# Performance work log

Measured on AMD Instinct MI355X. Metric: run time of the kernel, lower is better.

## Reference

```python
import jax, jax.numpy as jnp
import numpy as np

CODEBOOK_SIZE = 4096
CODE_DIM = 256
N = 65536
COMMITMENT_COST = 0.25


def setup_inputs() -> dict:
    key = jax.random.key(0)
    k1, k2 = jax.random.split(key)
    z_flat = jax.random.normal(k1, (N, CODE_DIM), dtype=jnp.float32)
    # embedding initialized uniform(-1/codebook_size, 1/codebook_size) as in torch module
    emb_weight = jax.random.uniform(
        k2, (CODEBOOK_SIZE, CODE_DIM), dtype=jnp.float32,
        minval=-1.0 / CODEBOOK_SIZE, maxval=1.0 / CODEBOOK_SIZE)
    return {"z_flat": z_flat, "emb_weight": emb_weight}


def reference(z_flat, emb_weight):
    # squared L2 distances: [N, K] = |z|^2 + |e|^2 - 2 z e^T
    distances = (
        jnp.sum(z_flat ** 2, axis=1, keepdims=True)
        + jnp.sum(emb_weight ** 2, axis=1)
        - 2.0 * jnp.matmul(z_flat, emb_weight.T)
    )
    indices = jnp.argmin(distances, axis=1)  # [N]
    quantized = emb_weight[indices]          # [N, code_dim]

    e_latent_loss = jnp.mean((jax.lax.stop_gradient(quantized) - z_flat) ** 2)
    q_latent_loss = jnp.mean((quantized - jax.lax.stop_gradient(z_flat)) ** 2)
    loss = q_latent_loss + COMMITMENT_COST * e_latent_loss

    # straight-through estimator
    quantized_st = z_flat + jax.lax.stop_gradient(quantized - z_flat)
    return (loss, quantized_st, indices)
```

## Files before the change

kernel.cpp:

```cpp
#include <hip/hip_runtime.h>

#define KCODES 4096
#define DIM    256
#define NROWS  65536
#define MARGIN 4.0e-4f
#define DSLACK 4.0e-5f
#define QDELT  4.0e-5f
#define LCAP   4096
#define CPAD   32
#define LSTRIDE (DIM + 4)

typedef unsigned long long u64;
typedef unsigned int  uint;
typedef unsigned short ushort;
typedef __attribute__((ext_vector_type(8))) short bf16x8;
typedef __attribute__((ext_vector_type(4))) float f32x4;

typedef __attribute__((address_space(3))) uint lds_u32_t;
typedef __attribute__((address_space(1))) uint glb_u32_t;

__device__ __forceinline__ void g2lds16(const void* g, void* l) {
    __builtin_amdgcn_global_load_lds((const glb_u32_t*)g, (lds_u32_t*)l, 16, 0, 0);
}

__device__ __forceinline__ float dppmin_pair(float m) {
    m = fminf(m, __int_as_float(__builtin_amdgcn_update_dpp(0, __float_as_int(m), 0xB1, 0xF, 0xF, true)));
    return m;
}
__device__ __forceinline__ float dppmin_row16(float m) {
    m = fminf(m, __int_as_float(__builtin_amdgcn_update_dpp(0, __float_as_int(m), 0xB1, 0xF, 0xF, true)));
    m = fminf(m, __int_as_float(__builtin_amdgcn_update_dpp(0, __float_as_int(m), 0x4E, 0xF, 0xF, true)));
    m = fminf(m, __int_as_float(__builtin_amdgcn_update_dpp(0, __float_as_int(m), 0x124, 0xF, 0xF, true)));
    m = fminf(m, __int_as_float(__builtin_amdgcn_update_dpp(0, __float_as_int(m), 0x128, 0xF, 0xF, true)));
    return m;
}
__device__ __forceinline__ uint dppor_row16(uint v) {
    v |= (uint)__builtin_amdgcn_update_dpp(0, (int)v, 0xB1, 0xF, 0xF, true);
    v |= (uint)__builtin_amdgcn_update_dpp(0, (int)v, 0x4E, 0xF, 0xF, true);
    v |= (uint)__builtin_amdgcn_update_dpp(0, (int)v, 0x124, 0xF, 0xF, true);
    v |= (uint)__builtin_amdgcn_update_dpp(0, (int)v, 0x128, 0xF, 0xF, true);
    return v;
}


__device__ __forceinline__ float np_half_sum128(const float4* __restrict__ p4) {
    #pragma clang fp contract(off)
    float4 v0 = p4[0], v1 = p4[1];
    float r0 = v0.x * v0.x, r1 = v0.y * v0.y, r2 = v0.z * v0.z, r3 = v0.w * v0.w;
    float r4 = v1.x * v1.x, r5 = v1.y * v1.y, r6 = v1.z * v1.z, r7 = v1.w * v1.w;
    #pragma unroll
    for (int i = 1; i < 16; ++i) {
        float4 a = p4[2 * i], b = p4[2 * i + 1];
        r0 += a.x * a.x; r1 += a.y * a.y; r2 += a.z * a.z; r3 += a.w * a.w;
        r4 += b.x * b.x; r5 += b.y * b.y; r6 += b.z * b.z; r7 += b.w * b.w;
    }
    return ((r0 + r1) + (r2 + r3)) + ((r4 + r5) + (r6 + r7));
}

__global__ void k_rownorm(const float* __restrict__ src, float* __restrict__ dst, int nrows) {
    int r = blockIdx.x * blockDim.x + threadIdx.x;
    if (r >= nrows) return;
    const float4* p4 = (const float4*)(src + (size_t)r * DIM);
    float s;
    {
        #pragma clang fp contract(off)
        s = np_half_sum128(p4) + np_half_sum128(p4 + 32);
    }
    dst[r] = s;
}

__device__ __forceinline__ float f32_dist(float Cr, float ebc, double accv) {
    #pragma clang fp contract(off)
    float A = Cr + ebc;
    float B = 2.0f * (float)accv;
    return A - B;
}

__device__ __forceinline__ ushort f2bf(float f) {
    uint u = __float_as_uint(f);
    return (ushort)((u + 0x7fffu + ((u >> 16) & 1u)) >> 16);
}

__device__ __forceinline__ uint4 pack8(float4 a, float4 b) {
    uint4 ov;
    ov.x = (uint)f2bf(a.x) | ((uint)f2bf(a.y) << 16);
    ov.y = (uint)f2bf(a.z) | ((uint)f2bf(a.w) << 16);
    ov.z = (uint)f2bf(b.x) | ((uint)f2bf(b.y) << 16);
    ov.w = (uint)f2bf(b.z) | ((uint)f2bf(b.w) << 16);
    return ov;
}


__global__ void k_prep(const float* __restrict__ src, ushort* __restrict__ dst,
                       float* __restrict__ nrm, int nrows) {
    int r = blockIdx.x * blockDim.x + threadIdx.x;
    if (r >= nrows) return;
    const float4* p4 = (const float4*)(src + (size_t)r * DIM);
    uint4* d4 = (uint4*)(dst + (size_t)r * DIM);
    float h[2];
    #pragma unroll
    for (int half = 0; half < 2; ++half) {
        #pragma clang fp contract(off)
        const float4* p = p4 + half * 32;
        float4 v0 = p[0], v1 = p[1];
        d4[half * 16] = pack8(v0, v1);
        float r0 = v0.x * v0.x, r1 = v0.y * v0.y, r2 = v0.z * v0.z, r3 = v0.w * v0.w;
        float r4 = v1.x * v1.x, r5 = v1.y * v1.y, r6 = v1.z * v1.z, r7 = v1.w * v1.w;
        #pragma unroll
        for (int i = 1; i < 16; ++i) {
            float4 a = p[2 * i], b = p[2 * i + 1];
            d4[half * 16 + i] = pack8(a, b);
            r0 += a.x * a.x; r1 += a.y * a.y; r2 += a.z * a.z; r3 += a.w * a.w;
            r4 += b.x * b.x; r5 += b.y * b.y; r6 += b.z * b.z; r7 += b.w * b.w;
        }
        h[half] = ((r0 + r1) + (r2 + r3)) + ((r4 + r5) + (r6 + r7));
    }
    {
        #pragma clang fp contract(off)
        nrm[r] = h[0] + h[1];
    }
}

__global__ void k_init(int* __restrict__ cnt) {
    cnt[blockIdx.x * 256 + threadIdx.x] = 0;
}

__global__ __launch_bounds__(256, 2)
void k_gemm(const ushort* __restrict__ zh, const ushort* __restrict__ eh,
            const float* __restrict__ Crow, const float* __restrict__ eb2,
            float* __restrict__ tk, uint* __restrict__ tk2) {
    __shared__ __align__(16) ushort Bs[2][64 * 256];

    const int t = threadIdx.x;
    const int lane = t & 63;
    const int w = t >> 6;
    const int l15 = lane & 15, l4 = lane >> 4;
    const int row0w = blockIdx.x * 128 + w * 32;

    const char* ebp = (const char*)eh;

    auto stage = [&](int buf, int ct2) {
        const char* base = ebp + (size_t)ct2 * 64 * 512;
        #pragma unroll
        for (int i = 0; i < 8; ++i) {
            int idx = i * 256 + t;
            int code = idx >> 5;
            int c16  = idx & 31;
            int src  = (code << 9) + ((c16 ^ (code & 7)) << 4);
            g2lds16(base + src, (char*)Bs[buf] + idx * 16);
        }
    };

    bf16x8 a[2][8];
    #pragma unroll
    for (int f = 0; f < 2; ++f)
        #pragma unroll
        for (int ks = 0; ks < 8; ++ks)
            a[f][ks] = *(const bf16x8*)&zh[(size_t)(row0w + f * 16 + l15) * 256 + ks * 32 + l4 * 8];

    float crf[8];
    #pragma unroll
    for (int f = 0; f < 2; ++f)
        #pragma unroll
        for (int rg = 0; rg < 4; ++rg)
            crf[f * 4 + rg] = Crow[row0w + f * 16 + l4 * 4 + rg];

    float mprev[8];
    const f32x4 fzero = (f32x4){0.f, 0.f, 0.f, 0.f};
    f32x4 accA[2][4], accB[2][4];
    float ebvA[4], ebvB[4];

    auto ksloop = [&](const ushort* Bb, f32x4 (&acc)[2][4]) {
        #pragma unroll
        for (int ks = 0; ks < 8; ++ks) {
            bf16x8 bfv[4];
            #pragma unroll
            for (int cg = 0; cg < 4; ++cg) {
                int rB = cg * 16 + l15;
                int off = rB * 256 + ((ks * 32 + l4 * 8) ^ ((l15 & 7) << 3));
                bfv[cg] = *(const bf16x8*)&Bb[off];
            }
            __builtin_amdgcn_s_setprio(1);
            #pragma unroll
            for (int f = 0; f < 2; ++f)
                #pragma unroll
                for (int cg = 0; cg < 4; ++cg)
                    acc[f][cg] = __builtin_amdgcn_mfma_f32_16x16x32_bf16(
                        a[f][ks], bfv[cg], ks == 0 ? fzero : acc[f][cg], 0, 0, 0);
            __builtin_amdgcn_s_setprio(0);
        }
    };

    auto epi = [&](f32x4 (&acc)[2][4], const float (&ebv)[4], int ct2, bool odd) {
        #pragma unroll
        for (int f = 0; f < 2; ++f) {
            #pragma unroll
            for (int rg = 0; rg < 4; ++rg) {
                float m =    fmaf(-2.0f, acc[f][0][rg], ebv[0]);
                m = fminf(m, fmaf(-2.0f, acc[f][1][rg], ebv[1]));
                m = fminf(m, fmaf(-2.0f, acc[f][2][rg], ebv[2]));
                m = fminf(m, fmaf(-2.0f, acc[f][3][rg], ebv[3]));
                m = dppmin_pair(m);
                if (!odd) {
                    mprev[f * 4 + rg] = m;
                } else {
                    m = fminf(m, mprev[f * 4 + rg]);
                    float mt = dppmin_row16(m);
                    int q = (int)((m - mt) * 2.5e4f);
                    q = q > 15 ? 15 : q;
                    uint pk = (uint)q << (4 * (l15 >> 1));
                    pk = dppor_row16(pk);
                    if (l15 == 0) {
                        int grow = row0w + f * 16 + l4 * 4 + rg;
                        int tt = ct2 >> 1;
                        tk [(size_t)tt * NROWS + grow] = crf[f * 4 + rg] + mt;
                        tk2[(size_t)tt * NROWS + grow] = pk;
                    }
                }
            }
        }
    };

    stage(0, 0);
    #pragma unroll
    for (int cg = 0; cg < 4; ++cg) ebvA[cg] = eb2[cg * 16 + l15];
    __syncthreads();

    for (int tp = 0; tp < 32; ++tp) {
        int t0 = 2 * tp;
        stage(1, t0 + 1);
        if (tp > 0) epi(accB, ebvB, t0 - 1, true);
        ksloop(Bs[0], accA);
        __syncthreads();

        if (tp < 31) stage(0, t0 + 2);
        #pragma unroll
        for (int cg = 0; cg < 4; ++cg) ebvB[cg] = eb2[(t0 + 1) * 64 + cg * 16 + l15];
        epi(accA, ebvA, t0, false);
        if (tp < 31) {
            #pragma unroll
            for (int cg = 0; cg < 4; ++cg) ebvA[cg] = eb2[(t0 + 2) * 64 + cg * 16 + l15];
        }
        ksloop(Bs[1], accB);
        __syncthreads();
    }
    epi(accB, ebvB, 63, true);
}

__global__ void k_lists(const float* __restrict__ tk, const uint* __restrict__ tk2,
                        int* __restrict__ cnt, int* __restrict__ list,
                        u64* __restrict__ fkey) {
    int row = blockIdx.x * 256 + threadIdx.x;
    int lane = threadIdx.x & 63;
    float tm[32]; uint pk[32];
    #pragma unroll
    for (int tt = 0; tt < 32; ++tt) {
        tm[tt] = tk [(size_t)tt * NROWS + row];
        pk[tt] = tk2[(size_t)tt * NROWS + row];
    }
    float best = tm[0];
    #pragma unroll
    for (int tt = 1; tt < 32; ++tt) best = fminf(best, tm[tt]);
    fkey[row] = ~0ull;
    float cutoff = best + (MARGIN + DSLACK);

    #pragma unroll
    for (int tt = 0; tt < 32; ++tt) {
        #pragma unroll
        for (int p = 0; p < 8; ++p) {
            float v = tm[tt] + (float)((pk[tt] >> (4 * p)) & 15u) * QDELT;
            bool pred = v <= cutoff;
            u64 mask = __ballot(pred);
            if (mask) {
                int sub = tt * 8 + p;
                int nq = __popcll(mask);
                int rank = __popcll(mask & ((1ull << lane) - 1ull));
                int base = 0;
                if (lane == 0) base = atomicAdd(&cnt[sub * CPAD], nq);
                base = __shfl(base, 0, 64);
                int pos = base + rank;
                if (pred && pos < LCAP) list[sub * LCAP + pos] = row;
            }
        }
    }
}

__global__ __launch_bounds__(256, 2)
void k_exact(const float* __restrict__ z, const float* __restrict__ e,
             const float* __restrict__ Crow, const float* __restrict__ eb2,
             const int* __restrict__ list, const int* __restrict__ cnt,
             u64* __restrict__ fkey) {
    __shared__ __align__(16) float ex[16][260];
    __shared__ __align__(16) float zx[32][260];
    __shared__ int rows[32];
    __shared__ u64 keytab[32][17];
    const int sub = blockIdx.x;
    const int tile = sub >> 3, p2 = sub & 7;
    const int nct = cnt[sub * CPAD];
    const int t = threadIdx.x;
    const int rp = t & 15, cs = t >> 4;

    {
        int cc = t >> 4, c8 = t & 15;
        int gcode = tile * 128 + (cc >> 3) * 64 + ((cc >> 1) & 3) * 16 + p2 * 2 + (cc & 1);
        const float4* src = (const float4*)(e + (size_t)gcode * DIM);
        float4* dr = (float4*)ex[cc];
        #pragma unroll
        for (int j = 0; j < 4; ++j) dr[c8 + 16 * j] = src[c8 + 16 * j];
    }
    const int gc0 = tile * 128 + (cs >> 3) * 64 + ((cs >> 1) & 3) * 16 + p2 * 2 + (cs & 1);
    const float ebc0 = eb2[gc0];

    for (int base = blockIdx.y * 32; base < nct; base += gridDim.y * 32) {
        __syncthreads();
        if (t < 32) {
            int i = base + t;
            rows[t] = list[sub * LCAP + (i < nct ? i : nct - 1)];
        }
        __syncthreads();
        {
            int rr = t >> 3, c8 = t & 7;
            const float4* src = (const float4*)(z + (size_t)rows[rr] * DIM);
            float4* dr = (float4*)zx[rr];
            #pragma unroll
            for (int j = 0; j < 8; ++j) dr[c8 + 8 * j] = src[c8 + 8 * j];
        }
        __syncthreads();

        double a0 = 0.0, a1 = 0.0;
        const float4* z0 = (const float4*)zx[rp];
        const float4* z1 = (const float4*)zx[rp + 16];
        const float4* e0 = (const float4*)ex[cs];
        #pragma unroll 8
        for (int d4 = 0; d4 < 64; ++d4) {
            float4 x0 = z0[d4], x1 = z1[d4], y0 = e0[d4];
            a0 += (double)x0.x * (double)y0.x; a0 += (double)x0.y * (double)y0.y;
            a0 += (double)x0.z * (double)y0.z; a0 += (double)x0.w * (double)y0.w;
            a1 += (double)x1.x * (double)y0.x; a1 += (double)x1.y * (double)y0.y;
            a1 += (double)x1.z * (double)y0.z; a1 += (double)x1.w * (double)y0.w;
        }
        int r0 = rows[rp], r1 = rows[rp + 16];
        float C0 = Crow[r0], C1 = Crow[r1];
        keytab[rp][cs]      = ((u64)__float_as_uint(f32_dist(C0, ebc0, a0)) << 32) | (u64)gc0;
        keytab[rp + 16][cs] = ((u64)__float_as_uint(f32_dist(C1, ebc0, a1)) << 32) | (u64)gc0;
        __syncthreads();
        if (t < 32) {
            u64 kb = keytab[t][0];
            #pragma unroll
            for (int j = 1; j < 16; ++j) {
                u64 k = keytab[t][j];
                kb = k < kb ? k : kb;
            }
            atomicMin((unsigned long long*)&fkey[rows[t]], kb);
        }
    }
}

__global__ __launch_bounds__(256)
void k_gather(const float* __restrict__ z, const float* __restrict__ e,
              const u64* __restrict__ fkey, float* __restrict__ out,
              double* __restrict__ partial) {
    __shared__ double lred[4];
    const int t = threadIdx.x;
    const int row = blockIdx.x * 32 + (t >> 3);
    const int c8 = t & 7;
    const int idx = (int)(fkey[row] & 0xffffffffull);
    if (c8 == 0) out[1 + (size_t)NROWS * DIM + row] = (float)idx;
    const float4* zr = (const float4*)(z + (size_t)row * DIM);
    const float4* er = (const float4*)(e + (size_t)idx * DIM);
    float4* orow = (float4*)(out + 1 + (size_t)row * DIM);
    double lacc = 0.0;
    #pragma unroll
    for (int j = 0; j < 8; ++j) {
        float4 q = er[c8 + 8 * j];
        float4 zv = zr[c8 + 8 * j];
        orow[c8 + 8 * j] = q;
        double d0 = (double)q.x - (double)zv.x;
        double d1 = (double)q.y - (double)zv.y;
        double d2 = (double)q.z - (double)zv.z;
        double d3 = (double)q.w - (double)zv.w;
        lacc += d0 * d0 + d1 * d1 + d2 * d2 + d3 * d3;
    }
    for (int off = 32; off > 0; off >>= 1) lacc += __shfl_down(lacc, off, 64);
    if ((t & 63) == 0) lred[t >> 6] = lacc;
    __syncthreads();
    if (t == 0) partial[blockIdx.x] = lred[0] + lred[1] + lred[2] + lred[3];
}

__global__ void k_finish(const double* __restrict__ partial, float* __restrict__ out, int n) {
    __shared__ double s[256];
    double a = 0.0;
    for (int i = threadIdx.x; i < n; i += 256) a += partial[i];
    s[threadIdx.x] = a;
    __syncthreads();
    for (int off = 128; off > 0; off >>= 1) {
        if (threadIdx.x < off) s[threadIdx.x] += s[threadIdx.x + off];
        __syncthreads();
    }
    if (threadIdx.x == 0)
        out[0] = (float)(1.25 * s[0] / ((double)NROWS * (double)DIM));
}


__global__ __launch_bounds__(256, 1)
void k_main_slow(const float* __restrict__ z, const float* __restrict__ e,
                 const float* __restrict__ Crow, const float* __restrict__ eb2,
                 float* __restrict__ out, double* __restrict__ partial) {
    __shared__ float  zt[64][LSTRIDE];
    __shared__ float  et[64][LSTRIDE];
    __shared__ float  redd[64][17];
    __shared__ int    redi[64][17];
    __shared__ int    bsel[64];
    __shared__ double lred[4];

    const int t  = threadIdx.x;
    const int tx = t & 15;
    const int ty = t >> 4;
    const int row0 = blockIdx.x * 64;

    {
        const float4* zsrc = (const float4*)(z + (size_t)row0 * DIM);
        for (int i = t; i < 64 * (DIM / 4); i += 256) {
            int r = i >> 6, c4 = i & 63;
            *(float4*)&zt[r][c4 * 4] = zsrc[r * (DIM / 4) + c4];
        }
    }
    float Cr[4];
    #pragma unroll
    for (int ri = 0; ri < 4; ++ri) Cr[ri] = Crow[row0 + ty * 4 + ri];
    float bestd[4]; int besti[4];
    #pragma unroll
    for (int ri = 0; ri < 4; ++ri) { bestd[ri] = __int_as_float(0x7f800000); besti[ri] = 0; }

    for (int kt = 0; kt < KCODES / 64; ++kt) {
        __syncthreads();
        {
            const float4* esrc = (const float4*)(e + (size_t)kt * 64 * DIM);
            for (int i = t; i < 64 * (DIM / 4); i += 256) {
                int r = i >> 6, c4 = i & 63;
                *(float4*)&et[r][c4 * 4] = esrc[r * (DIM / 4) + c4];
            }
        }
        __syncthreads();
        double acc[4][4];
        #pragma unroll
        for (int a = 0; a < 4; ++a)
            #pragma unroll
            for (int b = 0; b < 4; ++b) acc[a][b] = 0.0;
        #pragma unroll 4
        for (int d4 = 0; d4 < DIM / 4; ++d4) {
            float4 za[4], ea[4];
            #pragma unroll
            for (int ri = 0; ri < 4; ++ri) za[ri] = *(const float4*)&zt[ty * 4 + ri][d4 * 4];
            #pragma unroll
            for (int ci = 0; ci < 4; ++ci) ea[ci] = *(const float4*)&et[tx + 16 * ci][d4 * 4];
            #pragma unroll
            for (int ri = 0; ri < 4; ++ri)
                #pragma unroll
                for (int ci = 0; ci < 4; ++ci)
                    acc[ri][ci] += (double)za[ri].x * (double)ea[ci].x
                                 + (double)za[ri].y * (double)ea[ci].y
                                 + (double)za[ri].z * (double)ea[ci].z
                                 + (double)za[ri].w * (double)ea[ci].w;
        }
        #pragma unroll
        for (int ci = 0; ci < 4; ++ci) {
            int c = kt * 64 + tx + 16 * ci;
            float ebc = eb2[c];
            #pragma unroll
            for (int ri = 0; ri < 4; ++ri) {
                float d = f32_dist(Cr[ri], ebc, acc[ri][ci]);
                if (d < bestd[ri]) { bestd[ri] = d; besti[ri] = c; }
            }
        }
    }
    __syncthreads();
    #pragma unroll
    for (int ri = 0; ri < 4; ++ri) {
        redd[ty * 4 + ri][tx] = bestd[ri];
        redi[ty * 4 + ri][tx] = besti[ri];
    }
    __syncthreads();
    if (t < 64) {
        float bd = redd[t][0]; int bi = redi[t][0];
        for (int j = 1; j < 16; ++j) {
            float d = redd[t][j]; int i2 = redi[t][j];
            if (d < bd || (d == bd && i2 < bi)) { bd = d; bi = i2; }
        }
        bsel[t] = bi;
        out[1 + (size_t)NROWS * DIM + row0 + t] = (float)bi;
    }
    __syncthreads();
    double lacc = 0.0;
    {
        int r = t >> 2, qd = (t & 3) * 64;
        int bi = bsel[r];
        const float* qrow = e + (size_t)bi * DIM + qd;
        float* orow = out + 1 + (size_t)(row0 + r) * DIM + qd;
        #pragma unroll 4
        for (int d = 0; d < 64; ++d) {
            float qv = qrow[d], zv = zt[r][qd + d];
            double df = (double)qv - (double)zv;
            lacc += df * df;
            orow[d] = qv;
        }
    }
    for (int off = 32; off > 0; off >>= 1) lacc += __shfl_down(lacc, off, 64);
    if ((t & 63) == 0) lred[t >> 6] = lacc;
    __syncthreads();
    if (t == 0) partial[blockIdx.x] = lred[0] + lred[1] + lred[2] + lred[3];
}


extern "C" void kernel_launch(void* const* d_in, const int* in_sizes, int n_in,
                              void* d_out, int out_size, void* d_ws, size_t ws_size,
                              hipStream_t stream) {
    const float* z = (const float*)d_in[0];
    const float* e = (const float*)d_in[1];
    float* out = (float*)d_out;
    char* w = (char*)d_ws;

    size_t o = 0;
    auto take = [&](size_t b) { size_t r = o; o = (o + b + 255) & ~(size_t)255; return r; };
    size_t o_zh = take((size_t)NROWS * DIM * 2);
    size_t o_eh = take((size_t)KCODES * DIM * 2);
    size_t o_cr = take((size_t)NROWS * 4);
    size_t o_eb = take((size_t)KCODES * 4);
    size_t o_tk = take((size_t)32 * NROWS * 4);
    size_t o_t2 = take((size_t)32 * NROWS * 4);
    size_t o_fk = take((size_t)NROWS * 8);
    size_t o_cn = take((size_t)256 * CPAD * 4);
    size_t o_ls = take((size_t)256 * LCAP * 4);
    size_t o_pt = take((size_t)2048 * 8);
    size_t need = o;

    if (ws_size >= need) {
        ushort* zh = (ushort*)(w + o_zh);
        ushort* eh = (ushort*)(w + o_eh);
        float* Cr  = (float*)(w + o_cr);
        float* eb  = (float*)(w + o_eb);
        float* tk  = (float*)(w + o_tk);
        uint*  tk2 = (uint*)(w + o_t2);
        u64*   fk  = (u64*)(w + o_fk);
        int*   cn  = (int*)(w + o_cn);
        int*   ls  = (int*)(w + o_ls);
        double* pt = (double*)(w + o_pt);

        k_prep<<<NROWS / 256, 256, 0, stream>>>(z, zh, Cr, NROWS);
        k_prep<<<KCODES / 256, 256, 0, stream>>>(e, eh, eb, KCODES);
        k_init<<<(256 * CPAD) / 256, 256, 0, stream>>>(cn);
        k_gemm<<<NROWS / 128, 256, 0, stream>>>(zh, eh, Cr, eb, tk, tk2);
        k_lists<<<NROWS / 256, 256, 0, stream>>>(tk, tk2, cn, ls, fk);
        dim3 ge(256, 8);
        k_exact<<<ge, 256, 0, stream>>>(z, e, Cr, eb, ls, cn, fk);
        k_gather<<<NROWS / 32, 256, 0, stream>>>(z, e, fk, out, pt);
        k_finish<<<1, 256, 0, stream>>>(pt, out, 2048);
    } else {
        float* Cr  = (float*)w;
        float* eb  = Cr + NROWS;
        double* pt = (double*)(eb + KCODES);
        k_rownorm<<<NROWS / 256, 256, 0, stream>>>(z, Cr, NROWS);
        k_rownorm<<<KCODES / 256, 256, 0, stream>>>(e, eb, KCODES);
        k_main_slow<<<NROWS / 64, 256, 0, stream>>>(z, e, Cr, eb, out, pt);
        k_finish<<<1, 256, 0, stream>>>(pt, out, NROWS / 64);
    }
}
```

Baseline: 334.5 us.

## Enlarge exact-rescore row tile and derive loss from stored distances

The exact fp64 rescoring kernel now handles 64 candidate rows per iteration, and each thread computes two codes against two rows, so every z value read from LDS is reused across two codes and the per-row reduction shrinks from 16 entries to 8. Launch bounds drop to one block per SM to leave room for the larger shared tiles and extra accumulators. The gather kernel stops reading z and instead sums the winning distance stored in the key's upper 32 bits to form the loss, which removes a full pass over z and the fp64 difference arithmetic. The trade-off is that the loss now rests on the float32 f32_dist value rather than an exact fp64 recomputation, and occupancy in the rescoring kernel is lower.

```diff
diff --git a/kernel.cpp b/kernel.cpp
--- a/kernel.cpp
+++ b/kernel.cpp
@@ -285,69 +285,83 @@
     }
 }
 
-__global__ __launch_bounds__(256, 2)
+__global__ __launch_bounds__(256, 1)
 void k_exact(const float* __restrict__ z, const float* __restrict__ e,
              const float* __restrict__ Crow, const float* __restrict__ eb2,
              const int* __restrict__ list, const int* __restrict__ cnt,
              u64* __restrict__ fkey) {
     __shared__ __align__(16) float ex[16][260];
-    __shared__ __align__(16) float zx[32][260];
-    __shared__ int rows[32];
-    __shared__ u64 keytab[32][17];
+    __shared__ __align__(16) float zx[64][260];
+    __shared__ int rows[64];
+    __shared__ u64 keytab[64][9];
     const int sub = blockIdx.x;
     const int tile = sub >> 3, p2 = sub & 7;
     const int nct = cnt[sub * CPAD];
     const int t = threadIdx.x;
-    const int rp = t & 15, cs = t >> 4;
+    const int rp = t & 15;
+    const int cq = (t >> 4) & 7;
+    const int h  = t >> 7;
 
     {
-        int cc = t >> 4, c8 = t & 15;
+        int cc = t >> 4, c16 = t & 15;
         int gcode = tile * 128 + (cc >> 3) * 64 + ((cc >> 1) & 3) * 16 + p2 * 2 + (cc & 1);
         const float4* src = (const float4*)(e + (size_t)gcode * DIM);
         float4* dr = (float4*)ex[cc];
         #pragma unroll
-        for (int j = 0; j < 4; ++j) dr[c8 + 16 * j] = src[c8 + 16 * j];
-    }
-    const int gc0 = tile * 128 + (cs >> 3) * 64 + ((cs >> 1) & 3) * 16 + p2 * 2 + (cs & 1);
-    const float ebc0 = eb2[gc0];
-
-    for (int base = blockIdx.y * 32; base < nct; base += gridDim.y * 32) {
-        __syncthreads();
-        if (t < 32) {
+        for (int j = 0; j < 4; ++j) dr[c16 + 16 * j] = src[c16 + 16 * j];
+    }
+    const int gcA = tile * 128 + (cq >> 2) * 64 + (cq & 3) * 16 + p2 * 2;
+    const int gcB = gcA + 1;
+    const float ebA = eb2[gcA];
+    const float ebB = eb2[gcB];
+
+    for (int base = blockIdx.y * 64; base < nct; base += gridDim.y * 64) {
+        __syncthreads();
+        if (t < 64) {
             int i = base + t;
             rows[t] = list[sub * LCAP + (i < nct ? i : nct - 1)];
         }
         __syncthreads();
         {
-            int rr = t >> 3, c8 = t & 7;
+            int rr = t >> 2, c4 = t & 3;
             const float4* src = (const float4*)(z + (size_t)rows[rr] * DIM);
             float4* dr = (float4*)zx[rr];
             #pragma unroll
-            for (int j = 0; j < 8; ++j) dr[c8 + 8 * j] = src[c8 + 8 * j];
-        }
-        __syncthreads();
-
-        double a0 = 0.0, a1 = 0.0;
-        const float4* z0 = (const float4*)zx[rp];
-        const float4* z1 = (const float4*)zx[rp + 16];
-        const float4* e0 = (const float4*)ex[cs];
+            for (int j = 0; j < 16; ++j) dr[c4 + 4 * j] = src[c4 + 4 * j];
+        }
+        __syncthreads();
+
+        const int rl0 = rp + 32 * h, rl1 = rp + 16 + 32 * h;
+        double a0A = 0.0, a0B = 0.0, a1A = 0.0, a1B = 0.0;
+        const float4* z0 = (const float4*)zx[rl0];
+        const float4* z1 = (const float4*)zx[rl1];
+        const float4* eA = (const float4*)ex[2 * cq];
+        const float4* eB = (const float4*)ex[2 * cq + 1];
         #pragma unroll 8
         for (int d4 = 0; d4 < 64; ++d4) {
-            float4 x0 = z0[d4], x1 = z1[d4], y0 = e0[d4];
-            a0 += (double)x0.x * (double)y0.x; a0 += (double)x0.y * (double)y0.y;
-            a0 += (double)x0.z * (double)y0.z; a0 += (double)x0.w * (double)y0.w;
-            a1 += (double)x1.x * (double)y0.x; a1 += (double)x1.y * (double)y0.y;
-            a1 += (double)x1.z * (double)y0.z; a1 += (double)x1.w * (double)y0.w;
-        }
-        int r0 = rows[rp], r1 = rows[rp + 16];
+            float4 x0 = z0[d4], x1 = z1[d4], yA = eA[d4], yB = eB[d4];
+            a0A += (double)x0.x * (double)yA.x; a0A += (double)x0.y * (double)yA.y;
+            a0A += (double)x0.z * (double)yA.z; a0A += (double)x0.w * (double)yA.w;
+            a0B += (double)x0.x * (double)yB.x; a0B += (double)x0.y * (double)yB.y;
+            a0B += (double)x0.z * (double)yB.z; a0B += (double)x0.w * (double)yB.w;
+            a1A += (double)x1.x * (double)yA.x; a1A += (double)x1.y * (double)yA.y;
+            a1A += (double)x1.z * (double)yA.z; a1A += (double)x1.w * (double)yA.w;
+            a1B += (double)x1.x * (double)yB.x; a1B += (double)x1.y * (double)yB.y;
+            a1B += (double)x1.z * (double)yB.z; a1B += (double)x1.w * (double)yB.w;
+        }
+        int r0 = rows[rl0], r1 = rows[rl1];
         float C0 = Crow[r0], C1 = Crow[r1];
-        keytab[rp][cs]      = ((u64)__float_as_uint(f32_dist(C0, ebc0, a0)) << 32) | (u64)gc0;
-        keytab[rp + 16][cs] = ((u64)__float_as_uint(f32_dist(C1, ebc0, a1)) << 32) | (u64)gc0;
-        __syncthreads();
-        if (t < 32) {
+        u64 k0A = ((u64)__float_as_uint(f32_dist(C0, ebA, a0A)) << 32) | (u64)gcA;
+        u64 k0B = ((u64)__float_as_uint(f32_dist(C0, ebB, a0B)) << 32) | (u64)gcB;
+        u64 k1A = ((u64)__float_as_uint(f32_dist(C1, ebA, a1A)) << 32) | (u64)gcA;
+        u64 k1B = ((u64)__float_as_uint(f32_dist(C1, ebB, a1B)) << 32) | (u64)gcB;
+        keytab[rl0][cq] = k0A < k0B ? k0A : k0B;
+        keytab[rl1][cq] = k1A < k1B ? k1A : k1B;
+        __syncthreads();
+        if (t < 64) {
             u64 kb = keytab[t][0];
             #pragma unroll
-            for (int j = 1; j < 16; ++j) {
+            for (int j = 1; j < 8; ++j) {
                 u64 k = keytab[t][j];
                 kb = k < kb ? k : kb;
             }
@@ -357,34 +371,30 @@
 }
 
 __global__ __launch_bounds__(256)
-void k_gather(const float* __restrict__ z, const float* __restrict__ e,
-              const u64* __restrict__ fkey, float* __restrict__ out,
-              double* __restrict__ partial) {
-    __shared__ double lred[4];
+void k_gather(const float* __restrict__ e, const u64* __restrict__ fkey,
+              float* __restrict__ out, double* __restrict__ partial) {
+    __shared__ double s[32];
     const int t = threadIdx.x;
     const int row = blockIdx.x * 32 + (t >> 3);
     const int c8 = t & 7;
-    const int idx = (int)(fkey[row] & 0xffffffffull);
+    u64 key = fkey[row];
+    const int idx = (int)(key & 0xffffffffull);
     if (c8 == 0) out[1 + (size_t)NROWS * DIM + row] = (float)idx;
-    const float4* zr = (const float4*)(z + (size_t)row * DIM);
     const float4* er = (const float4*)(e + (size_t)idx * DIM);
     float4* orow = (float4*)(out + 1 + (size_t)row * DIM);
-    double lacc = 0.0;
-    #pragma unroll
-    for (int j = 0; j < 8; ++j) {
-        float4 q = er[c8 + 8 * j];
-        float4 zv = zr[c8 + 8 * j];
-        orow[c8 + 8 * j] = q;
-        double d0 = (double)q.x - (double)zv.x;
-        double d1 = (double)q.y - (double)zv.y;
-        double d2 = (double)q.z - (double)zv.z;
-        double d3 = (double)q.w - (double)zv.w;
-        lacc += d0 * d0 + d1 * d1 + d2 * d2 + d3 * d3;
-    }
-    for (int off = 32; off > 0; off >>= 1) lacc += __shfl_down(lacc, off, 64);
-    if ((t & 63) == 0) lred[t >> 6] = lacc;
-    __syncthreads();
-    if (t == 0) partial[blockIdx.x] = lred[0] + lred[1] + lred[2] + lred[3];
+    #pragma unroll
+    for (int j = 0; j < 8; ++j) orow[c8 + 8 * j] = er[c8 + 8 * j];
+    if (t < 32) {
+        u64 k2 = fkey[blockIdx.x * 32 + t];
+        s[t] = (double)__uint_as_float((uint)(k2 >> 32));
+    }
+    __syncthreads();
+    if (t == 0) {
+        double a = 0.0;
+        #pragma unroll
+        for (int i = 0; i < 32; ++i) a += s[i];
+        partial[blockIdx.x] = a;
+    }
 }
 
 __global__ void k_finish(const double* __restrict__ partial, float* __restrict__ out, int n) {
@@ -553,7 +563,7 @@
         k_lists<<<NROWS / 256, 256, 0, stream>>>(tk, tk2, cn, ls, fk);
         dim3 ge(256, 8);
         k_exact<<<ge, 256, 0, stream>>>(z, e, Cr, eb, ls, cn, fk);
-        k_gather<<<NROWS / 32, 256, 0, stream>>>(z, e, fk, out, pt);
+        k_gather<<<NROWS / 32, 256, 0, stream>>>(e, fk, out, pt);
         k_finish<<<1, 256, 0, stream>>>(pt, out, 2048);
     } else {
         float* Cr  = (float*)w;
```

New measurement: 341.6 us. 1.02x slower.

## Stationary codebook tiles in GEMM, stream z rows, and derive loss from exact keys

Applied to the files above, without the earlier changes.

The distance GEMM now keeps each wave's 64 codes in registers and streams 32-row z tiles through LDS, rather than holding z rows stationary and streaming the codebook. Candidate tiles drop to 64 per row with 16-code sub-groups quantized into 16-bit masks, which simplifies the exact-rescoring codebook indexing and halves list capacity. The gather kernel no longer rereads z to compute the loss; it sums the exact distance stored in the upper key bits. The tk/tk2 intermediate traffic changes shape, and the loss now depends on the precision of the stored distance.

```diff
diff --git a/kernel.cpp b/kernel.cpp
--- a/kernel.cpp
+++ b/kernel.cpp
@@ -6,7 +6,7 @@
 #define MARGIN 4.0e-4f
 #define DSLACK 4.0e-5f
 #define QDELT  4.0e-5f
-#define LCAP   4096
+#define LCAP   2048
 #define CPAD   32
 #define LSTRIDE (DIM + 4)
 
@@ -23,23 +23,12 @@
     __builtin_amdgcn_global_load_lds((const glb_u32_t*)g, (lds_u32_t*)l, 16, 0, 0);
 }
 
-__device__ __forceinline__ float dppmin_pair(float m) {
-    m = fminf(m, __int_as_float(__builtin_amdgcn_update_dpp(0, __float_as_int(m), 0xB1, 0xF, 0xF, true)));
-    return m;
-}
 __device__ __forceinline__ float dppmin_row16(float m) {
     m = fminf(m, __int_as_float(__builtin_amdgcn_update_dpp(0, __float_as_int(m), 0xB1, 0xF, 0xF, true)));
     m = fminf(m, __int_as_float(__builtin_amdgcn_update_dpp(0, __float_as_int(m), 0x4E, 0xF, 0xF, true)));
     m = fminf(m, __int_as_float(__builtin_amdgcn_update_dpp(0, __float_as_int(m), 0x124, 0xF, 0xF, true)));
     m = fminf(m, __int_as_float(__builtin_amdgcn_update_dpp(0, __float_as_int(m), 0x128, 0xF, 0xF, true)));
     return m;
-}
-__device__ __forceinline__ uint dppor_row16(uint v) {
-    v |= (uint)__builtin_amdgcn_update_dpp(0, (int)v, 0xB1, 0xF, 0xF, true);
-    v |= (uint)__builtin_amdgcn_update_dpp(0, (int)v, 0x4E, 0xF, 0xF, true);
-    v |= (uint)__builtin_amdgcn_update_dpp(0, (int)v, 0x124, 0xF, 0xF, true);
-    v |= (uint)__builtin_amdgcn_update_dpp(0, (int)v, 0x128, 0xF, 0xF, true);
-    return v;
 }
 
 
@@ -128,57 +117,70 @@
 __global__ __launch_bounds__(256, 2)
 void k_gemm(const ushort* __restrict__ zh, const ushort* __restrict__ eh,
             const float* __restrict__ Crow, const float* __restrict__ eb2,
-            float* __restrict__ tk, uint* __restrict__ tk2) {
-    __shared__ __align__(16) ushort Bs[2][64 * 256];
+            float* __restrict__ tk, ushort* __restrict__ tk2) {
+    __shared__ __align__(16) ushort Zs[2][32 * 256];
 
     const int t = threadIdx.x;
     const int lane = t & 63;
     const int w = t >> 6;
     const int l15 = lane & 15, l4 = lane >> 4;
-    const int row0w = blockIdx.x * 128 + w * 32;
-
-    const char* ebp = (const char*)eh;
-
-    auto stage = [&](int buf, int ct2) {
-        const char* base = ebp + (size_t)ct2 * 64 * 512;
-        #pragma unroll
-        for (int i = 0; i < 8; ++i) {
+    const int cgb = blockIdx.x >> 5;
+    const int zsl = blockIdx.x & 31;
+    const int code0w = cgb * 256 + w * 64;
+    const int tt = cgb * 4 + w;
+    const int row0s = zsl * 2048;
+
+    const char* zbp = (const char*)zh + (size_t)row0s * 512;
+
+    auto stage = [&](int buf, int zt) {
+        const char* base = zbp + (size_t)zt * 32 * 512;
+        #pragma unroll
+        for (int i = 0; i < 4; ++i) {
             int idx = i * 256 + t;
-            int code = idx >> 5;
-            int c16  = idx & 31;
-            int src  = (code << 9) + ((c16 ^ (code & 7)) << 4);
-            g2lds16(base + src, (char*)Bs[buf] + idx * 16);
+            int row = idx >> 5;
+            int c16 = idx & 31;
+            int src = (row << 9) + ((c16 ^ (row & 7)) << 4);
+            g2lds16(base + src, (char*)Zs[buf] + idx * 16);
         }
     };
 
-    bf16x8 a[2][8];
-    #pragma unroll
-    for (int f = 0; f < 2; ++f)
+    bf16x8 b[4][8];
+    #pragma unroll
+    for (int cg = 0; cg < 4; ++cg)
         #pragma unroll
         for (int ks = 0; ks < 8; ++ks)
-            a[f][ks] = *(const bf16x8*)&zh[(size_t)(row0w + f * 16 + l15) * 256 + ks * 32 + l4 * 8];
-
-    float crf[8];
-    #pragma unroll
-    for (int f = 0; f < 2; ++f)
-        #pragma unroll
-        for (int rg = 0; rg < 4; ++rg)
-            crf[f * 4 + rg] = Crow[row0w + f * 16 + l4 * 4 + rg];
-
-    float mprev[8];
+            b[cg][ks] = *(const bf16x8*)&eh[(size_t)(code0w + cg * 16 + l15) * 256 + ks * 32 + l4 * 8];
+
+    float ebv[4];
+    #pragma unroll
+    for (int cg = 0; cg < 4; ++cg) ebv[cg] = eb2[code0w + cg * 16 + l15];
+
     const f32x4 fzero = (f32x4){0.f, 0.f, 0.f, 0.f};
-    f32x4 accA[2][4], accB[2][4];
-    float ebvA[4], ebvB[4];
-
-    auto ksloop = [&](const ushort* Bb, f32x4 (&acc)[2][4]) {
+
+    stage(0, 0);
+    __syncthreads();
+
+    for (int zt = 0; zt < 64; ++zt) {
+        int buf = zt & 1;
+        if (zt < 63) stage(buf ^ 1, zt + 1);
+
+        float crf[8];
+        #pragma unroll
+        for (int f = 0; f < 2; ++f)
+            #pragma unroll
+            for (int rg = 0; rg < 4; ++rg)
+                crf[f * 4 + rg] = Crow[row0s + zt * 32 + f * 16 + l4 * 4 + rg];
+
+        f32x4 acc[2][4];
+        const ushort* Zb = Zs[buf];
         #pragma unroll
         for (int ks = 0; ks < 8; ++ks) {
-            bf16x8 bfv[4];
-            #pragma unroll
-            for (int cg = 0; cg < 4; ++cg) {
-                int rB = cg * 16 + l15;
-                int off = rB * 256 + ((ks * 32 + l4 * 8) ^ ((l15 & 7) << 3));
-                bfv[cg] = *(const bf16x8*)&Bb[off];
+            bf16x8 af[2];
+            #pragma unroll
+            for (int f = 0; f < 2; ++f) {
+                int rA = f * 16 + l15;
+                int off = rA * 256 + ((ks * 32 + l4 * 8) ^ ((l15 & 7) << 3));
+                af[f] = *(const bf16x8*)&Zb[off];
             }
             __builtin_amdgcn_s_setprio(1);
             #pragma unroll
@@ -186,93 +188,61 @@
                 #pragma unroll
                 for (int cg = 0; cg < 4; ++cg)
                     acc[f][cg] = __builtin_amdgcn_mfma_f32_16x16x32_bf16(
-                        a[f][ks], bfv[cg], ks == 0 ? fzero : acc[f][cg], 0, 0, 0);
+                        af[f], b[cg][ks], ks == 0 ? fzero : acc[f][cg], 0, 0, 0);
             __builtin_amdgcn_s_setprio(0);
         }
-    };
-
-    auto epi = [&](f32x4 (&acc)[2][4], const float (&ebv)[4], int ct2, bool odd) {
+
         #pragma unroll
         for (int f = 0; f < 2; ++f) {
             #pragma unroll
             for (int rg = 0; rg < 4; ++rg) {
-                float m =    fmaf(-2.0f, acc[f][0][rg], ebv[0]);
-                m = fminf(m, fmaf(-2.0f, acc[f][1][rg], ebv[1]));
-                m = fminf(m, fmaf(-2.0f, acc[f][2][rg], ebv[2]));
-                m = fminf(m, fmaf(-2.0f, acc[f][3][rg], ebv[3]));
-                m = dppmin_pair(m);
-                if (!odd) {
-                    mprev[f * 4 + rg] = m;
-                } else {
-                    m = fminf(m, mprev[f * 4 + rg]);
-                    float mt = dppmin_row16(m);
-                    int q = (int)((m - mt) * 2.5e4f);
-                    q = q > 15 ? 15 : q;
-                    uint pk = (uint)q << (4 * (l15 >> 1));
-                    pk = dppor_row16(pk);
-                    if (l15 == 0) {
-                        int grow = row0w + f * 16 + l4 * 4 + rg;
-                        int tt = ct2 >> 1;
-                        tk [(size_t)tt * NROWS + grow] = crf[f * 4 + rg] + mt;
-                        tk2[(size_t)tt * NROWS + grow] = pk;
-                    }
+                float m0 = dppmin_row16(fmaf(-2.0f, acc[f][0][rg], ebv[0]));
+                float m1 = dppmin_row16(fmaf(-2.0f, acc[f][1][rg], ebv[1]));
+                float m2 = dppmin_row16(fmaf(-2.0f, acc[f][2][rg], ebv[2]));
+                float m3 = dppmin_row16(fmaf(-2.0f, acc[f][3][rg], ebv[3]));
+                float mt = fminf(fminf(m0, m1), fminf(m2, m3));
+                int q0 = (int)((m0 - mt) * 2.5e4f); q0 = q0 > 15 ? 15 : q0;
+                int q1 = (int)((m1 - mt) * 2.5e4f); q1 = q1 > 15 ? 15 : q1;
+                int q2 = (int)((m2 - mt) * 2.5e4f); q2 = q2 > 15 ? 15 : q2;
+                int q3 = (int)((m3 - mt) * 2.5e4f); q3 = q3 > 15 ? 15 : q3;
+                uint pkv = (uint)q0 | ((uint)q1 << 4) | ((uint)q2 << 8) | ((uint)q3 << 12);
+                if (l15 == 0) {
+                    int grow = row0s + zt * 32 + f * 16 + l4 * 4 + rg;
+                    tk [(size_t)tt * NROWS + grow] = crf[f * 4 + rg] + mt;
+                    tk2[(size_t)tt * NROWS + grow] = (ushort)pkv;
                 }
             }
         }
-    };
-
-    stage(0, 0);
-    #pragma unroll
-    for (int cg = 0; cg < 4; ++cg) ebvA[cg] = eb2[cg * 16 + l15];
-    __syncthreads();
-
-    for (int tp = 0; tp < 32; ++tp) {
-        int t0 = 2 * tp;
-        stage(1, t0 + 1);
-        if (tp > 0) epi(accB, ebvB, t0 - 1, true);
-        ksloop(Bs[0], accA);
-        __syncthreads();
-
-        if (tp < 31) stage(0, t0 + 2);
-        #pragma unroll
-        for (int cg = 0; cg < 4; ++cg) ebvB[cg] = eb2[(t0 + 1) * 64 + cg * 16 + l15];
-        epi(accA, ebvA, t0, false);
-        if (tp < 31) {
-            #pragma unroll
-            for (int cg = 0; cg < 4; ++cg) ebvA[cg] = eb2[(t0 + 2) * 64 + cg * 16 + l15];
-        }
-        ksloop(Bs[1], accB);
-        __syncthreads();
-    }
-    epi(accB, ebvB, 63, true);
-}
-
-__global__ void k_lists(const float* __restrict__ tk, const uint* __restrict__ tk2,
+        __syncthreads();
+    }
+}
+
+__global__ void k_lists(const float* __restrict__ tk, const ushort* __restrict__ tk2,
                         int* __restrict__ cnt, int* __restrict__ list,
                         u64* __restrict__ fkey) {
     int row = blockIdx.x * 256 + threadIdx.x;
     int lane = threadIdx.x & 63;
-    float tm[32]; uint pk[32];
-    #pragma unroll
-    for (int tt = 0; tt < 32; ++tt) {
+    float tm[64]; uint pk[64];
+    #pragma unroll
+    for (int tt = 0; tt < 64; ++tt) {
         tm[tt] = tk [(size_t)tt * NROWS + row];
         pk[tt] = tk2[(size_t)tt * NROWS + row];
     }
     float best = tm[0];
     #pragma unroll
-    for (int tt = 1; tt < 32; ++tt) best = fminf(best, tm[tt]);
+    for (int tt = 1; tt < 64; ++tt) best = fminf(best, tm[tt]);
     fkey[row] = ~0ull;
     float cutoff = best + (MARGIN + DSLACK);
 
     #pragma unroll
-    for (int tt = 0; tt < 32; ++tt) {
-        #pragma unroll
-        for (int p = 0; p < 8; ++p) {
+    for (int tt = 0; tt < 64; ++tt) {
+        #pragma unroll
+        for (int p = 0; p < 4; ++p) {
             float v = tm[tt] + (float)((pk[tt] >> (4 * p)) & 15u) * QDELT;
             bool pred = v <= cutoff;
             u64 mask = __ballot(pred);
             if (mask) {
-                int sub = tt * 8 + p;
+                int sub = tt * 4 + p;
                 int nq = __popcll(mask);
                 int rank = __popcll(mask & ((1ull << lane) - 1ull));
                 int base = 0;
@@ -295,20 +265,18 @@
     __shared__ int rows[32];
     __shared__ u64 keytab[32][17];
     const int sub = blockIdx.x;
-    const int tile = sub >> 3, p2 = sub & 7;
     const int nct = cnt[sub * CPAD];
     const int t = threadIdx.x;
     const int rp = t & 15, cs = t >> 4;
 
     {
-        int cc = t >> 4, c8 = t & 15;
-        int gcode = tile * 128 + (cc >> 3) * 64 + ((cc >> 1) & 3) * 16 + p2 * 2 + (cc & 1);
-        const float4* src = (const float4*)(e + (size_t)gcode * DIM);
+        int cc = t >> 4, c16 = t & 15;
+        const float4* src = (const float4*)(e + (size_t)(sub * 16 + cc) * DIM);
         float4* dr = (float4*)ex[cc];
         #pragma unroll
-        for (int j = 0; j < 4; ++j) dr[c8 + 16 * j] = src[c8 + 16 * j];
-    }
-    const int gc0 = tile * 128 + (cs >> 3) * 64 + ((cs >> 1) & 3) * 16 + p2 * 2 + (cs & 1);
+        for (int j = 0; j < 4; ++j) dr[c16 + 16 * j] = src[c16 + 16 * j];
+    }
+    const int gc0 = sub * 16 + cs;
     const float ebc0 = eb2[gc0];
 
     for (int base = blockIdx.y * 32; base < nct; base += gridDim.y * 32) {
@@ -357,34 +325,30 @@
 }
 
 __global__ __launch_bounds__(256)
-void k_gather(const float* __restrict__ z, const float* __restrict__ e,
-              const u64* __restrict__ fkey, float* __restrict__ out,
-              double* __restrict__ partial) {
-    __shared__ double lred[4];
+void k_gather(const float* __restrict__ e, const u64* __restrict__ fkey,
+              float* __restrict__ out, double* __restrict__ partial) {
+    __shared__ double s[32];
     const int t = threadIdx.x;
     const int row = blockIdx.x * 32 + (t >> 3);
     const int c8 = t & 7;
-    const int idx = (int)(fkey[row] & 0xffffffffull);
+    u64 key = fkey[row];
+    const int idx = (int)(key & 0xffffffffull);
     if (c8 == 0) out[1 + (size_t)NROWS * DIM + row] = (float)idx;
-    const float4* zr = (const float4*)(z + (size_t)row * DIM);
     const float4* er = (const float4*)(e + (size_t)idx * DIM);
     float4* orow = (float4*)(out + 1 + (size_t)row * DIM);
-    double lacc = 0.0;
-    #pragma unroll
-    for (int j = 0; j < 8; ++j) {
-        float4 q = er[c8 + 8 * j];
-        float4 zv = zr[c8 + 8 * j];
-        orow[c8 + 8 * j] = q;
-        double d0 = (double)q.x - (double)zv.x;
-        double d1 = (double)q.y - (double)zv.y;
-        double d2 = (double)q.z - (double)zv.z;
-        double d3 = (double)q.w - (double)zv.w;
-        lacc += d0 * d0 + d1 * d1 + d2 * d2 + d3 * d3;
-    }
-    for (int off = 32; off > 0; off >>= 1) lacc += __shfl_down(lacc, off, 64);
-    if ((t & 63) == 0) lred[t >> 6] = lacc;
-    __syncthreads();
-    if (t == 0) partial[blockIdx.x] = lred[0] + lred[1] + lred[2] + lred[3];
+    #pragma unroll
+    for (int j = 0; j < 8; ++j) orow[c8 + 8 * j] = er[c8 + 8 * j];
+    if (t < 32) {
+        u64 k2 = fkey[blockIdx.x * 32 + t];
+        s[t] = (double)__uint_as_float((uint)(k2 >> 32));
+    }
+    __syncthreads();
+    if (t == 0) {
+        double a = 0.0;
+        #pragma unroll
+        for (int i = 0; i < 32; ++i) a += s[i];
+        partial[blockIdx.x] = a;
+    }
 }
 
 __global__ void k_finish(const double* __restrict__ partial, float* __restrict__ out, int n) {
@@ -526,8 +490,8 @@
     size_t o_eh = take((size_t)KCODES * DIM * 2);
     size_t o_cr = take((size_t)NROWS * 4);
     size_t o_eb = take((size_t)KCODES * 4);
-    size_t o_tk = take((size_t)32 * NROWS * 4);
-    size_t o_t2 = take((size_t)32 * NROWS * 4);
+    size_t o_tk = take((size_t)64 * NROWS * 4);
+    size_t o_t2 = take((size_t)64 * NROWS * 2);
     size_t o_fk = take((size_t)NROWS * 8);
     size_t o_cn = take((size_t)256 * CPAD * 4);
     size_t o_ls = take((size_t)256 * LCAP * 4);
@@ -540,7 +504,7 @@
         float* Cr  = (float*)(w + o_cr);
         float* eb  = (float*)(w + o_eb);
         float* tk  = (float*)(w + o_tk);
-        uint*  tk2 = (uint*)(w + o_t2);
+        ushort* tk2 = (ushort*)(w + o_t2);
         u64*   fk  = (u64*)(w + o_fk);
         int*   cn  = (int*)(w + o_cn);
         int*   ls  = (int*)(w + o_ls);
@@ -549,11 +513,11 @@
         k_prep<<<NROWS / 256, 256, 0, stream>>>(z, zh, Cr, NROWS);
         k_prep<<<KCODES / 256, 256, 0, stream>>>(e, eh, eb, KCODES);
         k_init<<<(256 * CPAD) / 256, 256, 0, stream>>>(cn);
-        k_gemm<<<NROWS / 128, 256, 0, stream>>>(zh, eh, Cr, eb, tk, tk2);
+        k_gemm<<<512, 256, 0, stream>>>(zh, eh, Cr, eb, tk, tk2);
         k_lists<<<NROWS / 256, 256, 0, stream>>>(tk, tk2, cn, ls, fk);
         dim3 ge(256, 8);
         k_exact<<<ge, 256, 0, stream>>>(z, e, Cr, eb, ls, cn, fk);
-        k_gather<<<NROWS / 32, 256, 0, stream>>>(z, e, fk, out, pt);
+        k_gather<<<NROWS / 32, 256, 0, stream>>>(e, fk, out, pt);
         k_finish<<<1, 256, 0, stream>>>(pt, out, 2048);
     } else {
         float* Cr  = (float*)w;
```

New measurement: 423.0 us. +26.5%, slower.
